# Performance work log

Measured on AMD Instinct MI355X. Metric: run time of the kernel, lower is better.

## Reference

```python
import jax, jax.numpy as jnp
import numpy as np

B, S, D, H = 2, 2048, 1024, 16
DK = D // H
NEG = -1e9


def setup_inputs() -> dict:
    key = jax.random.key(0)
    ks = jax.random.split(key, 11)
    s = 1.0 / np.sqrt(D)
    inp = {
        "q": jax.random.normal(ks[0], (B, S, D), jnp.float32),
        "k": jax.random.normal(ks[1], (B, S, D), jnp.float32),
        "v": jax.random.normal(ks[2], (B, S, D), jnp.float32),
        "mask": jnp.tril(jnp.ones((S, S), jnp.int32))[None, None],  # [1,1,S,S] causal
        "Wq": jax.random.normal(ks[3], (D, D), jnp.float32) * s,
        "bq": jnp.zeros((D,), jnp.float32),
        "Wk": jax.random.normal(ks[4], (D, D), jnp.float32) * s,
        "bk": jnp.zeros((D,), jnp.float32),
        "Wv": jax.random.normal(ks[5], (D, D), jnp.float32) * s,
        "bv": jnp.zeros((D,), jnp.float32),
        "Wo": jax.random.normal(ks[6], (D, D), jnp.float32) * s,
        "bo": jnp.zeros((D,), jnp.float32),
    }
    return inp


def reference(q, k, v, mask, Wq, bq, Wk, bk, Wv, bv, Wo, bo):
    # projections (torch Linear: x @ W.T + b)
    Q = q @ Wq.T + bq
    K = k @ Wk.T + bk
    V = v @ Wv.T + bv
    # [B,S,D] -> [B,H,S,DK]
    Q = Q.reshape(B, S, H, DK).transpose(0, 2, 1, 3)
    K = K.reshape(B, S, H, DK).transpose(0, 2, 1, 3)
    V = V.reshape(B, S, H, DK).transpose(0, 2, 1, 3)
    scores = jnp.einsum("bhqd,bhkd->bhqk", Q, K) / jnp.sqrt(jnp.float32(DK))
    scores = jnp.where(mask == 0, jnp.float32(NEG), scores)
    attn = jax.nn.softmax(scores, axis=-1)  # dropout p=0.0 -> identity
    x = jnp.einsum("bhqk,bhkd->bhqd", attn, V)
    x = x.transpose(0, 2, 1, 3).reshape(B, S, D)
    return x @ Wo.T + bo
```

## Files before the change

kernel.cpp:

```cpp
#include <hip/hip_runtime.h>
#include <hip/hip_bf16.h>


typedef __bf16 bf16_t;
typedef __bf16 bf16x4 __attribute__((ext_vector_type(4)));
typedef __bf16 bf16x8 __attribute__((ext_vector_type(8)));
typedef float f32x4 __attribute__((ext_vector_type(4)));

#define BB 2
#define SS 2048
#define DD 1024
#define HH 16
#define DKK 64
#define MM 4096

#define NELT ((size_t)BB * SS * DD)
#define WELT ((size_t)DD * DD)

__device__ __align__(16) bf16_t g_ws[7 * NELT + 4 * WELT];

__device__ __forceinline__ void gld16(const bf16_t* g, bf16_t* l) {
    __builtin_amdgcn_global_load_lds(
        (const __attribute__((address_space(1))) void*)g,
        (__attribute__((address_space(3))) void*)l, 16, 0, 0);
}

__global__ __launch_bounds__(256) void cvt7(
    const float* __restrict__ q,  const float* __restrict__ k,  const float* __restrict__ v,
    const float* __restrict__ Wq, const float* __restrict__ Wk, const float* __restrict__ Wv,
    const float* __restrict__ Wo,
    bf16_t* __restrict__ qb, bf16_t* __restrict__ kb, bf16_t* __restrict__ vb,
    bf16_t* __restrict__ Wqb, bf16_t* __restrict__ Wkb, bf16_t* __restrict__ Wvb,
    bf16_t* __restrict__ Wob)
{
    const float* s; bf16_t* d; size_t n;
    switch (blockIdx.y) {
        case 0: s = q;  d = qb;  n = NELT; break;
        case 1: s = k;  d = kb;  n = NELT; break;
        case 2: s = v;  d = vb;  n = NELT; break;
        case 3: s = Wq; d = Wqb; n = WELT; break;
        case 4: s = Wk; d = Wkb; n = WELT; break;
        case 5: s = Wv; d = Wvb; n = WELT; break;
        default: s = Wo; d = Wob; n = WELT; break;
    }
    size_t e = ((size_t)blockIdx.x * 256 + threadIdx.x) * 8;
    if (e >= n) return;
    f32x4 a = *(const f32x4*)(s + e);
    f32x4 b = *(const f32x4*)(s + e + 4);
    bf16x8 o;
    #pragma unroll
    for (int i = 0; i < 4; ++i) { o[i] = (bf16_t)a[i]; o[4 + i] = (bf16_t)b[i]; }
    *(bf16x8*)(d + e) = o;
}

#define BM 128
#define BN 128
#define BKG 64
#define LDC 136

__global__ __launch_bounds__(256) void gemm_qkv3(
    const bf16_t* __restrict__ qb, const bf16_t* __restrict__ kb, const bf16_t* __restrict__ vb,
    const bf16_t* __restrict__ Wqb, const bf16_t* __restrict__ Wkb, const bf16_t* __restrict__ Wvb,
    const float* __restrict__ bq, const float* __restrict__ bk, const float* __restrict__ bv,
    bf16_t* __restrict__ Qp, bf16_t* __restrict__ Kp, bf16_t* __restrict__ Vt)
{
    const int z = blockIdx.z;
    const bf16_t* A    = (z == 0) ? qb  : (z == 1) ? kb  : vb;
    const bf16_t* W    = (z == 0) ? Wqb : (z == 1) ? Wkb : Wvb;
    const float*  bias = (z == 0) ? bq  : (z == 1) ? bk  : bv;

    __shared__ __align__(16) bf16_t smem[128 * LDC];
    bf16_t (*As)[BKG] = (bf16_t(*)[BKG])smem;
    bf16_t (*Bs)[BKG] = (bf16_t(*)[BKG])(smem + 128 * BKG);
    bf16_t (*Ct)[LDC] = (bf16_t(*)[LDC])smem;

    const int tid  = threadIdx.x;
    const int wave = tid >> 6;
    const int lane = tid & 63;
    const int quad = lane >> 4;
    const int c16  = lane & 15;
    const int bm = blockIdx.x * BM;
    const int bn = blockIdx.y * BN;
    const int wm = (wave >> 1) * 64;
    const int wn = (wave & 1) * 64;

    const int srow = lane >> 3;
    const int scol = (lane & 7) * 8;

    f32x4 acc[4][4] = {};

    for (int k0 = 0; k0 < DD; k0 += BKG) {
        __syncthreads();
        #pragma unroll
        for (int j = 0; j < 4; ++j) {
            int r0 = wave * 32 + j * 8;
            gld16(A + (size_t)(bm + r0 + srow) * DD + k0 + scol, &As[r0][0]);
            gld16(W + (size_t)(bn + r0 + srow) * DD + k0 + scol, &Bs[r0][0]);
        }
        __syncthreads();

        #pragma unroll
        for (int ks = 0; ks < 2; ++ks) {
            bf16x8 af[4], bfr[4];
            #pragma unroll
            for (int tm = 0; tm < 4; ++tm)
                af[tm] = *(const bf16x8*)(&As[wm + tm * 16 + c16][ks * 32 + quad * 8]);
            #pragma unroll
            for (int tn = 0; tn < 4; ++tn)
                bfr[tn] = *(const bf16x8*)(&Bs[wn + tn * 16 + c16][ks * 32 + quad * 8]);
            #pragma unroll
            for (int tm = 0; tm < 4; ++tm)
                #pragma unroll
                for (int tn = 0; tn < 4; ++tn)
                    acc[tm][tn] = __builtin_amdgcn_mfma_f32_16x16x32_bf16(
                        af[tm], bfr[tn], acc[tm][tn], 0, 0, 0);
        }
    }

    float bia[4];
    #pragma unroll
    for (int tn = 0; tn < 4; ++tn)
        bia[tn] = bias[bn + wn + tn * 16 + c16];

    if (z < 2) {
        const float osc = (z == 0) ? 0.125f : 1.0f;
        bf16_t* C = (z == 0) ? Qp : Kp;
        #pragma unroll
        for (int tm = 0; tm < 4; ++tm)
            #pragma unroll
            for (int r = 0; r < 4; ++r) {
                size_t base = (size_t)(bm + wm + tm * 16 + quad * 4 + r) * DD;
                #pragma unroll
                for (int tn = 0; tn < 4; ++tn)
                    C[base + bn + wn + tn * 16 + c16] =
                        (bf16_t)((acc[tm][tn][r] + bia[tn]) * osc);
            }
    } else {
        __syncthreads();
        #pragma unroll
        for (int tm = 0; tm < 4; ++tm)
            #pragma unroll
            for (int tn = 0; tn < 4; ++tn) {
                bf16x4 pk;
                #pragma unroll
                for (int r = 0; r < 4; ++r)
                    pk[r] = (bf16_t)(acc[tm][tn][r] + bia[tn]);
                *(bf16x4*)(&Ct[wn + tn * 16 + c16][wm + tm * 16 + quad * 4]) = pk;
            }
        __syncthreads();
        const int b_    = bm >> 11;
        const int sbase = bm & (SS - 1);
        #pragma unroll
        for (int p = 0; p < 4; ++p) {
            int col = p * 32 + (tid >> 3);
            int si  = (tid & 7) * 8;
            size_t rowoff = (size_t)(b_ * 1024 + bn + col) * SS + sbase;
            #pragma unroll
            for (int half = 0; half < 2; ++half) {
                int s = si + half * 64;
                *(bf16x8*)(&Vt[rowoff + s]) = *(const bf16x8*)(&Ct[col][s]);
            }
        }
    }
}

__global__ __launch_bounds__(256) void gemm_out(
    const bf16_t* __restrict__ A,
    const bf16_t* __restrict__ W,
    const float* __restrict__ bias,
    float* __restrict__ C)
{
    __shared__ __align__(16) bf16_t As[128][BKG];
    __shared__ __align__(16) bf16_t Bs[64][BKG];

    const int tid  = threadIdx.x;
    const int wave = tid >> 6;
    const int lane = tid & 63;
    const int quad = lane >> 4;
    const int c16  = lane & 15;
    const int bm = blockIdx.x * 128;
    const int bn = blockIdx.y * 64;
    const int wm = (wave >> 1) * 64;
    const int wn = (wave & 1) * 32;

    const int srow = lane >> 3;
    const int scol = (lane & 7) * 8;

    f32x4 acc[4][2] = {};

    for (int k0 = 0; k0 < DD; k0 += BKG) {
        __syncthreads();
        #pragma unroll
        for (int j = 0; j < 4; ++j) {
            int r0 = wave * 32 + j * 8;
            gld16(A + (size_t)(bm + r0 + srow) * DD + k0 + scol, &As[r0][0]);
        }
        #pragma unroll
        for (int j = 0; j < 2; ++j) {
            int r0 = wave * 16 + j * 8;
            gld16(W + (size_t)(bn + r0 + srow) * DD + k0 + scol, &Bs[r0][0]);
        }
        __syncthreads();

        #pragma unroll
        for (int ks = 0; ks < 2; ++ks) {
            bf16x8 af[4], bfr[2];
            #pragma unroll
            for (int tm = 0; tm < 4; ++tm)
                af[tm] = *(const bf16x8*)(&As[wm + tm * 16 + c16][ks * 32 + quad * 8]);
            #pragma unroll
            for (int tn = 0; tn < 2; ++tn)
                bfr[tn] = *(const bf16x8*)(&Bs[wn + tn * 16 + c16][ks * 32 + quad * 8]);
            #pragma unroll
            for (int tm = 0; tm < 4; ++tm)
                #pragma unroll
                for (int tn = 0; tn < 2; ++tn)
                    acc[tm][tn] = __builtin_amdgcn_mfma_f32_16x16x32_bf16(
                        af[tm], bfr[tn], acc[tm][tn], 0, 0, 0);
        }
    }

    float bia[2];
    #pragma unroll
    for (int tn = 0; tn < 2; ++tn)
        bia[tn] = bias[bn + wn + tn * 16 + c16];

    #pragma unroll
    for (int tm = 0; tm < 4; ++tm)
        #pragma unroll
        for (int r = 0; r < 4; ++r) {
            size_t base = (size_t)(bm + wm + tm * 16 + quad * 4 + r) * DD;
            #pragma unroll
            for (int tn = 0; tn < 2; ++tn)
                C[base + bn + wn + tn * 16 + c16] = acc[tm][tn][r] + bia[tn];
        }
}

#define LDPS 40
#define LDOF 68

__global__ __launch_bounds__(256) void attn_fwd5(
    const bf16_t* __restrict__ Q,
    const bf16_t* __restrict__ K,
    const bf16_t* __restrict__ Vt,
    bf16_t* __restrict__ O)
{
    const int bh = blockIdx.y;
    const int b  = bh >> 4;
    const int h  = bh & 15;
    const int qt = (int)gridDim.x - 1 - blockIdx.x;
    const int qbase = qt * 32;
    const int U = qt + 1;
    const int wave = threadIdx.x >> 6;
    const int lane = threadIdx.x & 63;
    const int quad = lane >> 4;
    const int c16  = lane & 15;

    __shared__ __align__(16) unsigned char smraw[4 * 32 * LDOF * 4];
    bf16_t (*Ps)[32][LDPS] = (bf16_t(*)[32][LDPS])smraw;
    float  (*Of)[32][LDOF] = (float(*)[32][LDOF])smraw;
    __shared__ float Ls[4][32];

    bf16x8 qf[2][2];
    #pragma unroll
    for (int tm = 0; tm < 2; ++tm) {
        const bf16_t* qp = Q + ((size_t)b * SS + qbase + tm * 16 + c16) * DD + h * DKK;
        qf[tm][0] = *(const bf16x8*)(qp + quad * 8);
        qf[tm][1] = *(const bf16x8*)(qp + 32 + quad * 8);
    }

    const bf16_t* Kb = K  + (size_t)b * SS * DD + h * DKK;
    const bf16_t* Vb = Vt + (size_t)(b * 1024 + h * DKK) * SS;

    f32x4 oacc[2][4] = {};
    float lsum[2][4] = {};

    bf16x8 kfA[2][2], kfB[2][2];
    {
        int kb = wave * 32;
        #pragma unroll
        for (int ct = 0; ct < 2; ++ct) {
            const bf16_t* kp = Kb + (size_t)(kb + ct * 16 + c16) * DD;
            kfA[ct][0] = *(const bf16x8*)(kp + quad * 8);
            kfA[ct][1] = *(const bf16x8*)(kp + 32 + quad * 8);
        }
    }

    auto step = [&](int kb, bf16x8 (&kfc)[2][2], bf16x8 (&kfn)[2][2]) {
        f32x4 sc[2][2];
        #pragma unroll
        for (int tm = 0; tm < 2; ++tm)
            #pragma unroll
            for (int ct = 0; ct < 2; ++ct) {
                f32x4 s = {};
                s = __builtin_amdgcn_mfma_f32_16x16x32_bf16(qf[tm][0], kfc[ct][0], s, 0, 0, 0);
                s = __builtin_amdgcn_mfma_f32_16x16x32_bf16(qf[tm][1], kfc[ct][1], s, 0, 0, 0);
                sc[tm][ct] = s;
            }

        if (kb + 128 < U * 32) {
            #pragma unroll
            for (int ct = 0; ct < 2; ++ct) {
                const bf16_t* kp = Kb + (size_t)(kb + 128 + ct * 16 + c16) * DD;
                kfn[ct][0] = *(const bf16x8*)(kp + quad * 8);
                kfn[ct][1] = *(const bf16x8*)(kp + 32 + quad * 8);
            }
        }

        bf16x8 vf[4];
        #pragma unroll
        for (int tn = 0; tn < 4; ++tn)
            vf[tn] = *(const bf16x8*)(Vb + (size_t)(tn * 16 + c16) * SS + kb + quad * 8);

        const bool needmask = (kb >= qbase);
        #pragma unroll
        for (int tm = 0; tm < 2; ++tm) {
            int rbase = qbase + tm * 16 + quad * 4;
            #pragma unroll
            for (int ct = 0; ct < 2; ++ct) {
                int kidx = kb + ct * 16 + c16;
                #pragma unroll
                for (int r = 0; r < 4; ++r) {
                    float s = sc[tm][ct][r];
                    if (needmask && kidx > rbase + r) s = -1e9f;
                    float p = __expf(s);
                    Ps[wave][tm * 16 + quad * 4 + r][ct * 16 + c16] = (bf16_t)p;
                    lsum[tm][r] += p;
                }
            }
        }

        asm volatile("s_waitcnt lgkmcnt(0)" ::: "memory");

        #pragma unroll
        for (int tm = 0; tm < 2; ++tm) {
            bf16x8 pa = *(const bf16x8*)(&Ps[wave][tm * 16 + c16][quad * 8]);
            #pragma unroll
            for (int tn = 0; tn < 4; ++tn)
                oacc[tm][tn] = __builtin_amdgcn_mfma_f32_16x16x32_bf16(
                    pa, vf[tn], oacc[tm][tn], 0, 0, 0);
        }
    };

    {
        int u = wave; bool cur = false;
        while (u < U) {
            if (!cur) step(u * 32, kfA, kfB);
            else      step(u * 32, kfB, kfA);
            u += 4; cur = !cur;
        }
    }

    __syncthreads();

    #pragma unroll
    for (int tm = 0; tm < 2; ++tm)
        #pragma unroll
        for (int tn = 0; tn < 4; ++tn)
            #pragma unroll
            for (int r = 0; r < 4; ++r)
                Of[wave][tm * 16 + quad * 4 + r][tn * 16 + c16] = oacc[tm][tn][r];

    #pragma unroll
    for (int tm = 0; tm < 2; ++tm)
        #pragma unroll
        for (int r = 0; r < 4; ++r) {
            float l = lsum[tm][r];
            #pragma unroll
            for (int off = 1; off < 16; off <<= 1)
                l += __shfl_xor(l, off, 64);
            if (c16 == 0) Ls[wave][tm * 16 + quad * 4 + r] = l;
        }
    __syncthreads();

    {
        int row = wave * 8 + (lane >> 3);
        int col = (lane & 7) * 8;
        float l = Ls[0][row] + Ls[1][row] + Ls[2][row] + Ls[3][row];
        f32x4 s0 = {}, s1 = {};
        #pragma unroll
        for (int p = 0; p < 4; ++p) {
            s0 += *(const f32x4*)(&Of[p][row][col]);
            s1 += *(const f32x4*)(&Of[p][row][col + 4]);
        }
        float inv = 1.0f / l;
        bf16x8 o;
        #pragma unroll
        for (int i = 0; i < 4; ++i) {
            o[i]     = (bf16_t)(s0[i] * inv);
            o[4 + i] = (bf16_t)(s1[i] * inv);
        }
        *(bf16x8*)(&O[((size_t)b * SS + qbase + row) * DD + h * DKK + col]) = o;
    }
}

extern "C" void kernel_launch(void* const* d_in, const int* in_sizes, int n_in,
                              void* d_out, int out_size, void* d_ws, size_t ws_size,
                              hipStream_t stream) {
    (void)in_sizes; (void)n_in; (void)out_size; (void)d_ws; (void)ws_size;
    const float* q  = (const float*)d_in[0];
    const float* k  = (const float*)d_in[1];
    const float* v  = (const float*)d_in[2];
    const float* Wq = (const float*)d_in[4];
    const float* bq = (const float*)d_in[5];
    const float* Wk = (const float*)d_in[6];
    const float* bk = (const float*)d_in[7];
    const float* Wv = (const float*)d_in[8];
    const float* bv = (const float*)d_in[9];
    const float* Wo = (const float*)d_in[10];
    const float* bo = (const float*)d_in[11];

    bf16_t* ws;
    hipGetSymbolAddress((void**)&ws, HIP_SYMBOL(g_ws));
    bf16_t* Qp  = ws;
    bf16_t* Kp  = Qp + NELT;
    bf16_t* Vt  = Kp + NELT;
    bf16_t* Xa  = Vt + NELT;
    bf16_t* qb  = Xa + NELT;
    bf16_t* kb  = qb + NELT;
    bf16_t* vb  = kb + NELT;
    bf16_t* Wqb = vb + NELT;
    bf16_t* Wkb = Wqb + WELT;
    bf16_t* Wvb = Wkb + WELT;
    bf16_t* Wob = Wvb + WELT;

    cvt7<<<dim3(2048, 7), 256, 0, stream>>>(q, k, v, Wq, Wk, Wv, Wo,
                                            qb, kb, vb, Wqb, Wkb, Wvb, Wob);

    gemm_qkv3<<<dim3(MM / BM, DD / BN, 3), 256, 0, stream>>>(
        qb, kb, vb, Wqb, Wkb, Wvb, bq, bk, bv, Qp, Kp, Vt);

    attn_fwd5<<<dim3(SS / 32, BB * HH), 256, 0, stream>>>(Qp, Kp, Vt, Xa);

    gemm_out<<<dim3(MM / 128, DD / 64), 256, 0, stream>>>(Xa, Wob, bo, (float*)d_out);
}
```

Measured before the change: 314.4 us.

## Pair causal query tiles per block and transpose score MFMA for vectorized P stores

Attention now launches 1024 blocks, and each processes two query tiles (qt and 63-qt) so every block does the same amount of causal work. A flat block index mapping interleaves heads. Scores are computed as K·Qᵀ so each lane holds four consecutive keys and can write P with a single bf16x4 store, and the row-sum reduction needs fewer shuffles. The final cross-wave reduction uses a smaller LDS buffer in two halves, and launch bounds request 4 blocks per SM. The trade-off is more syncthreads and fewer total blocks.

```diff
diff --git a/kernel.cpp b/kernel.cpp
--- a/kernel.cpp
+++ b/kernel.cpp
@@ -237,160 +237,164 @@
 }
 
 #define LDPS 40
-#define LDOF 68
-
-__global__ __launch_bounds__(256) void attn_fwd5(
+#define LDCF 68
+
+__global__ __launch_bounds__(256, 4) void attn_fwd6(
     const bf16_t* __restrict__ Q,
     const bf16_t* __restrict__ K,
     const bf16_t* __restrict__ Vt,
     bf16_t* __restrict__ O)
 {
-    const int bh = blockIdx.y;
-    const int b  = bh >> 4;
-    const int h  = bh & 15;
-    const int qt = (int)gridDim.x - 1 - blockIdx.x;
-    const int qbase = qt * 32;
-    const int U = qt + 1;
+    const int flat = blockIdx.x;
+    const int bh   = (flat & 7) * 4 + (flat >> 8);
+    const int pair = (flat >> 3) & 31;
+    const int b = bh >> 4;
+    const int h = bh & 15;
+
     const int wave = threadIdx.x >> 6;
     const int lane = threadIdx.x & 63;
     const int quad = lane >> 4;
     const int c16  = lane & 15;
 
-    __shared__ __align__(16) unsigned char smraw[4 * 32 * LDOF * 4];
+    __shared__ __align__(16) unsigned char smraw[4 * 16 * LDCF * 4];
     bf16_t (*Ps)[32][LDPS] = (bf16_t(*)[32][LDPS])smraw;
-    float  (*Of)[32][LDOF] = (float(*)[32][LDOF])smraw;
+    float  (*Cf)[16][LDCF] = (float(*)[16][LDCF])smraw;
     __shared__ float Ls[4][32];
-
-    bf16x8 qf[2][2];
-    #pragma unroll
-    for (int tm = 0; tm < 2; ++tm) {
-        const bf16_t* qp = Q + ((size_t)b * SS + qbase + tm * 16 + c16) * DD + h * DKK;
-        qf[tm][0] = *(const bf16x8*)(qp + quad * 8);
-        qf[tm][1] = *(const bf16x8*)(qp + 32 + quad * 8);
-    }
 
     const bf16_t* Kb = K  + (size_t)b * SS * DD + h * DKK;
     const bf16_t* Vb = Vt + (size_t)(b * 1024 + h * DKK) * SS;
 
-    f32x4 oacc[2][4] = {};
-    float lsum[2][4] = {};
-
-    bf16x8 kfA[2][2], kfB[2][2];
-    {
-        int kb = wave * 32;
-        #pragma unroll
-        for (int ct = 0; ct < 2; ++ct) {
-            const bf16_t* kp = Kb + (size_t)(kb + ct * 16 + c16) * DD;
-            kfA[ct][0] = *(const bf16x8*)(kp + quad * 8);
-            kfA[ct][1] = *(const bf16x8*)(kp + 32 + quad * 8);
-        }
-    }
-
-    auto step = [&](int kb, bf16x8 (&kfc)[2][2], bf16x8 (&kfn)[2][2]) {
-        f32x4 sc[2][2];
-        #pragma unroll
-        for (int tm = 0; tm < 2; ++tm)
+    bf16_t*       pw = &Ps[wave][c16][quad * 4];
+    const bf16_t* pr = &Ps[wave][c16][quad * 8];
+
+    const int qts[2] = { 63 - pair, pair };
+
+    for (int t = 0; t < 2; ++t) {
+        const int qt    = qts[t];
+        const int qbase = qt * 32;
+        const int U     = qt + 1;
+        const int kend  = U * 32;
+
+        bf16x8 qf[2][2];
+        #pragma unroll
+        for (int tm = 0; tm < 2; ++tm) {
+            const bf16_t* qp = Q + ((size_t)b * SS + qbase + tm * 16 + c16) * DD + h * DKK;
+            qf[tm][0] = *(const bf16x8*)(qp + quad * 8);
+            qf[tm][1] = *(const bf16x8*)(qp + 32 + quad * 8);
+        }
+
+        f32x4 oacc[2][4] = {};
+        float lsum2[2] = {0.f, 0.f};
+
+        bf16x8 kfA[2][2], kfB[2][2];
+        {
+            int kb = wave * 32;
             #pragma unroll
             for (int ct = 0; ct < 2; ++ct) {
-                f32x4 s = {};
-                s = __builtin_amdgcn_mfma_f32_16x16x32_bf16(qf[tm][0], kfc[ct][0], s, 0, 0, 0);
-                s = __builtin_amdgcn_mfma_f32_16x16x32_bf16(qf[tm][1], kfc[ct][1], s, 0, 0, 0);
-                sc[tm][ct] = s;
-            }
-
-        if (kb + 128 < U * 32) {
-            #pragma unroll
-            for (int ct = 0; ct < 2; ++ct) {
-                const bf16_t* kp = Kb + (size_t)(kb + 128 + ct * 16 + c16) * DD;
-                kfn[ct][0] = *(const bf16x8*)(kp + quad * 8);
-                kfn[ct][1] = *(const bf16x8*)(kp + 32 + quad * 8);
-            }
-        }
-
-        bf16x8 vf[4];
-        #pragma unroll
-        for (int tn = 0; tn < 4; ++tn)
-            vf[tn] = *(const bf16x8*)(Vb + (size_t)(tn * 16 + c16) * SS + kb + quad * 8);
-
-        const bool needmask = (kb >= qbase);
+                const bf16_t* kp = Kb + (size_t)(kb + ct * 16 + c16) * DD;
+                kfA[ct][0] = *(const bf16x8*)(kp + quad * 8);
+                kfA[ct][1] = *(const bf16x8*)(kp + 32 + quad * 8);
+            }
+        }
+
+        auto step = [&](int kb, bf16x8 (&kfc)[2][2], bf16x8 (&kfn)[2][2]) {
+            f32x4 sc[2][2];
+            #pragma unroll
+            for (int tm = 0; tm < 2; ++tm)
+                #pragma unroll
+                for (int ct = 0; ct < 2; ++ct) {
+                    f32x4 s = {};
+                    s = __builtin_amdgcn_mfma_f32_16x16x32_bf16(kfc[ct][0], qf[tm][0], s, 0, 0, 0);
+                    s = __builtin_amdgcn_mfma_f32_16x16x32_bf16(kfc[ct][1], qf[tm][1], s, 0, 0, 0);
+                    sc[tm][ct] = s;
+                }
+
+            if (kb + 128 < kend) {
+                #pragma unroll
+                for (int ct = 0; ct < 2; ++ct) {
+                    const bf16_t* kp = Kb + (size_t)(kb + 128 + ct * 16 + c16) * DD;
+                    kfn[ct][0] = *(const bf16x8*)(kp + quad * 8);
+                    kfn[ct][1] = *(const bf16x8*)(kp + 32 + quad * 8);
+                }
+            }
+
+            bf16x8 vf[4];
+            #pragma unroll
+            for (int tn = 0; tn < 4; ++tn)
+                vf[tn] = *(const bf16x8*)(Vb + (size_t)(tn * 16 + c16) * SS + kb + quad * 8);
+
+            const bool needmask = (kb == qbase);
+            #pragma unroll
+            for (int tm = 0; tm < 2; ++tm) {
+                const int qrow = qbase + tm * 16 + c16;
+                #pragma unroll
+                for (int ct = 0; ct < 2; ++ct) {
+                    bf16x4 w;
+                    #pragma unroll
+                    for (int r = 0; r < 4; ++r) {
+                        float s = sc[tm][ct][r];
+                        if (needmask && (kb + ct * 16 + quad * 4 + r > qrow)) s = -1e9f;
+                        float p = __expf(s);
+                        lsum2[tm] += p;
+                        w[r] = (bf16_t)p;
+                    }
+                    *(bf16x4*)(pw + tm * 16 * LDPS + ct * 16) = w;
+                }
+            }
+
+            asm volatile("s_waitcnt lgkmcnt(0)" ::: "memory");
+
+            #pragma unroll
+            for (int tm = 0; tm < 2; ++tm) {
+                bf16x8 pa = *(const bf16x8*)(pr + tm * 16 * LDPS);
+                #pragma unroll
+                for (int tn = 0; tn < 4; ++tn)
+                    oacc[tm][tn] = __builtin_amdgcn_mfma_f32_16x16x32_bf16(
+                        pa, vf[tn], oacc[tm][tn], 0, 0, 0);
+            }
+        };
+
+        {
+            int u = wave; bool cur = false;
+            while (u < U) {
+                if (!cur) step(u * 32, kfA, kfB);
+                else      step(u * 32, kfB, kfA);
+                u += 4; cur = !cur;
+            }
+        }
+
         #pragma unroll
         for (int tm = 0; tm < 2; ++tm) {
-            int rbase = qbase + tm * 16 + quad * 4;
-            #pragma unroll
-            for (int ct = 0; ct < 2; ++ct) {
-                int kidx = kb + ct * 16 + c16;
-                #pragma unroll
-                for (int r = 0; r < 4; ++r) {
-                    float s = sc[tm][ct][r];
-                    if (needmask && kidx > rbase + r) s = -1e9f;
-                    float p = __expf(s);
-                    Ps[wave][tm * 16 + quad * 4 + r][ct * 16 + c16] = (bf16_t)p;
-                    lsum[tm][r] += p;
-                }
-            }
-        }
-
-        asm volatile("s_waitcnt lgkmcnt(0)" ::: "memory");
-
+            float l = lsum2[tm];
+            l += __shfl_xor(l, 16, 64);
+            l += __shfl_xor(l, 32, 64);
+            if (lane < 16) Ls[wave][tm * 16 + lane] = l;
+        }
+
+        const int row = threadIdx.x >> 4;
+        const int col = (threadIdx.x & 15) * 4;
         #pragma unroll
         for (int tm = 0; tm < 2; ++tm) {
-            bf16x8 pa = *(const bf16x8*)(&Ps[wave][tm * 16 + c16][quad * 8]);
+            __syncthreads();
             #pragma unroll
             for (int tn = 0; tn < 4; ++tn)
-                oacc[tm][tn] = __builtin_amdgcn_mfma_f32_16x16x32_bf16(
-                    pa, vf[tn], oacc[tm][tn], 0, 0, 0);
-        }
-    };
-
-    {
-        int u = wave; bool cur = false;
-        while (u < U) {
-            if (!cur) step(u * 32, kfA, kfB);
-            else      step(u * 32, kfB, kfA);
-            u += 4; cur = !cur;
-        }
-    }
-
-    __syncthreads();
-
-    #pragma unroll
-    for (int tm = 0; tm < 2; ++tm)
-        #pragma unroll
-        for (int tn = 0; tn < 4; ++tn)
-            #pragma unroll
-            for (int r = 0; r < 4; ++r)
-                Of[wave][tm * 16 + quad * 4 + r][tn * 16 + c16] = oacc[tm][tn][r];
-
-    #pragma unroll
-    for (int tm = 0; tm < 2; ++tm)
-        #pragma unroll
-        for (int r = 0; r < 4; ++r) {
-            float l = lsum[tm][r];
-            #pragma unroll
-            for (int off = 1; off < 16; off <<= 1)
-                l += __shfl_xor(l, off, 64);
-            if (c16 == 0) Ls[wave][tm * 16 + quad * 4 + r] = l;
-        }
-    __syncthreads();
-
-    {
-        int row = wave * 8 + (lane >> 3);
-        int col = (lane & 7) * 8;
-        float l = Ls[0][row] + Ls[1][row] + Ls[2][row] + Ls[3][row];
-        f32x4 s0 = {}, s1 = {};
-        #pragma unroll
-        for (int p = 0; p < 4; ++p) {
-            s0 += *(const f32x4*)(&Of[p][row][col]);
-            s1 += *(const f32x4*)(&Of[p][row][col + 4]);
-        }
-        float inv = 1.0f / l;
-        bf16x8 o;
-        #pragma unroll
-        for (int i = 0; i < 4; ++i) {
-            o[i]     = (bf16_t)(s0[i] * inv);
-            o[4 + i] = (bf16_t)(s1[i] * inv);
-        }
-        *(bf16x8*)(&O[((size_t)b * SS + qbase + row) * DD + h * DKK + col]) = o;
+                #pragma unroll
+                for (int r = 0; r < 4; ++r)
+                    Cf[wave][quad * 4 + r][tn * 16 + c16] = oacc[tm][tn][r];
+            __syncthreads();
+            f32x4 ssum = {};
+            #pragma unroll
+            for (int p = 0; p < 4; ++p)
+                ssum += *(const f32x4*)(&Cf[p][row][col]);
+            float l = Ls[0][tm * 16 + row] + Ls[1][tm * 16 + row]
+                    + Ls[2][tm * 16 + row] + Ls[3][tm * 16 + row];
+            float inv = 1.0f / l;
+            bf16x4 o;
+            #pragma unroll
+            for (int i = 0; i < 4; ++i) o[i] = (bf16_t)(ssum[i] * inv);
+            *(bf16x4*)(&O[((size_t)b * SS + qbase + tm * 16 + row) * DD + h * DKK + col]) = o;
+        }
+        __syncthreads();
     }
 }
 
@@ -430,7 +434,7 @@
     gemm_qkv3<<<dim3(MM / BM, DD / BN, 3), 256, 0, stream>>>(
         qb, kb, vb, Wqb, Wkb, Wvb, bq, bk, bv, Qp, Kp, Vt);
 
-    attn_fwd5<<<dim3(SS / 32, BB * HH), 256, 0, stream>>>(Qp, Kp, Vt, Xa);
+    attn_fwd6<<<dim3(1024), 256, 0, stream>>>(Qp, Kp, Vt, Xa);
 
     gemm_out<<<dim3(MM / 128, DD / 64), 256, 0, stream>>>(Xa, Wob, bo, (float*)d_out);
 }
```

After: 356.7 us. +13.5%, slower.
